# Optimization experiments

Hardware: AMD Instinct MI355X
Metric: run time of the kernel (lower is better)

## Reference

```python
import jax, jax.numpy as jnp
import numpy as np

DIM = 1024
HEADS = 16
DIM_HEAD = 64
INNER = HEADS * DIM_HEAD  # 1024
SCALE = DIM ** (-0.5)  # module scales by dim**-0.5 (not dim_head)


def setup_inputs() -> dict:
    key = jax.random.key(0)
    kx, kqkv, kwo, kbo = jax.random.split(key, 4)
    x = jax.random.normal(kx, (2, 2048, DIM), dtype=jnp.float32)
    W_qkv = jax.random.normal(kqkv, (DIM, 3 * INNER), dtype=jnp.float32) * (DIM ** -0.5)
    W_out = jax.random.normal(kwo, (INNER, DIM), dtype=jnp.float32) * (INNER ** -0.5)
    b_out = jax.random.normal(kbo, (DIM,), dtype=jnp.float32) * 0.01
    return {"x": x, "W_qkv": W_qkv, "W_out": W_out, "b_out": b_out}


def reference(x, W_qkv, W_out, b_out):
    b, n, _ = x.shape
    qkv = x @ W_qkv  # [b, n, 3*inner]
    q, k, v = jnp.split(qkv, 3, axis=-1)
    # [b, n, h*d] -> [b, h, n, d]
    reshape = lambda t: t.reshape(b, n, HEADS, DIM_HEAD).transpose(0, 2, 1, 3)
    q, k, v = reshape(q), reshape(k), reshape(v)
    dots = jnp.einsum('bhid,bhjd->bhij', q, k) * SCALE  # [b, h, n, n]
    attn = jax.nn.softmax(dots, axis=-1)
    out = jnp.einsum('bhij,bhjd->bhid', attn, v)  # [b, h, n, d]
    out = out.transpose(0, 2, 1, 3).reshape(b, n, INNER)
    return out @ W_out + b_out
```

## Files before the change

### kernel.cpp

```cpp
#include <hip/hip_runtime.h>

typedef __bf16 bf16x8 __attribute__((ext_vector_type(8)));
typedef __bf16 bf16x4 __attribute__((ext_vector_type(4)));
typedef __bf16 bf16x2 __attribute__((ext_vector_type(2)));
typedef float f32x4 __attribute__((ext_vector_type(4)));
typedef float f32x16 __attribute__((ext_vector_type(16)));
typedef int i32x4 __attribute__((ext_vector_type(4)));
typedef unsigned int u32x2 __attribute__((ext_vector_type(2)));

#define EXP2_SCALE 0.045084439f

__device__ __forceinline__ void async16(void* lds, const void* g) {
  __builtin_amdgcn_global_load_lds(
      (__attribute__((address_space(1))) unsigned int*)(g),
      (__attribute__((address_space(3))) unsigned int*)(lds), 16, 0, 0);
}

__device__ __forceinline__ unsigned int pack2(float a, float b) {
  bf16x2 t;
  t[0] = (__bf16)a;
  t[1] = (__bf16)b;
  return __builtin_bit_cast(unsigned int, t);
}

__device__ __forceinline__ float fexp2(float x) {
#if __has_builtin(__builtin_amdgcn_exp2f)
  return __builtin_amdgcn_exp2f(x);
#else
  return exp2f(x);
#endif
}

__device__ __forceinline__ void plswap(unsigned int& d, unsigned int& s) {
#if __has_builtin(__builtin_amdgcn_permlane32_swap)
  u32x2 r = __builtin_amdgcn_permlane32_swap(d, s, false, false);
  d = r[0];
  s = r[1];
#else
  asm("v_permlane32_swap_b32 %0, %1" : "+v"(d), "+v"(s));
#endif
}

__device__ __forceinline__ int detect_block(const unsigned short* win, int* cnt_sh) {
  if (threadIdx.x == 0) *cnt_sh = 0;
  __syncthreads();
  int c = 0;
#pragma unroll
  for (int j = 0; j < 8; j++) {
    const unsigned short u = win[threadIdx.x * 8 + j];
    if (((u >> 7) & 0xFF) >= 0xC0) c++;
  }
  if (c) atomicAdd(cnt_sh, c);
  __syncthreads();
  return (*cnt_sh >= 64) ? 1 : 0;
}

__global__ __launch_bounds__(256) void prep(
    const void* __restrict__ x, const void* __restrict__ Wqkv,
    const void* __restrict__ Wout, __bf16* __restrict__ xb,
    __bf16* __restrict__ WqkvT, __bf16* __restrict__ WoutT,
    int* __restrict__ flagp)
{
  __shared__ __bf16 tile[64 * 65];
  __shared__ int cnt;
  const int bx = blockIdx.x;
  const int t = threadIdx.x;

  if (bx < 2048) {
    const long base = (long)bx * 2048;
    const int f = detect_block((const unsigned short*)x + base, &cnt);
    if (bx == 0 && t == 0) *flagp = f;
    const long i = base + t * 8;
    if (f) {
      const f32x4* s4 = (const f32x4*)((const float*)x + i);
      const f32x4 v0 = s4[0], v1 = s4[1];
      bf16x8 o;
#pragma unroll
      for (int j = 0; j < 4; j++) o[j] = (__bf16)v0[j];
#pragma unroll
      for (int j = 0; j < 4; j++) o[4 + j] = (__bf16)v1[j];
      *(bf16x8*)&xb[i] = o;
    } else {
      *(bf16x8*)&xb[i] = *(const bf16x8*)((const __bf16*)x + i);
    }
    return;
  }

  const void* in;  __bf16* out;  int R = 1024, C, tcx, tr;
  if (bx < 2816) {
    const int idx = bx - 2048;
    in = Wqkv; out = WqkvT; C = 3072; tcx = (idx % 48) * 64; tr = (idx / 48) * 64;
  } else {
    const int idx = bx - 2816;
    in = Wout; out = WoutT; C = 1024; tcx = (idx % 16) * 64; tr = (idx / 16) * 64;
  }
  const int f = detect_block((const unsigned short*)in + (long)tr * C + tcx, &cnt);
#pragma unroll
  for (int i = 0; i < 16; i++) {
    const int idx = t + 256 * i;
    const int r = idx >> 6, c = idx & 63;
    const long g = (long)(tr + r) * C + tcx + c;
    tile[r * 65 + c] = f ? (__bf16)((const float*)in)[g] : ((const __bf16*)in)[g];
  }
  __syncthreads();
#pragma unroll
  for (int i = 0; i < 16; i++) {
    const int idx = t + 256 * i;
    const int r = idx >> 6, c = idx & 63;
    out[(long)(tcx + r) * R + tr + c] = tile[c * 65 + r];
  }
}

__global__ __launch_bounds__(256, 3) void gemm_qkv(
    const __bf16* __restrict__ A, const __bf16* __restrict__ Bt,
    __bf16* __restrict__ Qb, __bf16* __restrict__ Kc, __bf16* __restrict__ Vc)
{
  __shared__ __bf16 smem[17408];
  const int t = threadIdx.x;
  const int l = t & 63;
  const int w = t >> 6;
  const int wr = w >> 1, wc = w & 1;
  const int lid = blockIdx.y * 32 + blockIdx.x;
  const int s = (lid & 7) * 96 + (lid >> 3);
  const long m0 = (long)(s & 31) * 128;
  const long n0 = (long)(s >> 5) * 128;
  const int K = 1024;

  const int srow = w * 16 + (l >> 2);
  const int skof = (l & 3) * 8;
  const __bf16* gA = A + (m0 + srow) * (long)K + skof;
  const __bf16* gB = Bt + (n0 + srow) * (long)K + skof;
  const int Ao[2] = {0, 8192}, Bo[2] = {4096, 12288};
  const int lof = w * 512 + l * 8;

  async16(smem + Ao[0] + lof,        gA);
  async16(smem + Ao[0] + 2048 + lof, gA + 64 * (long)K);
  async16(smem + Bo[0] + lof,        gB);
  async16(smem + Bo[0] + 2048 + lof, gB + 64 * (long)K);
  gA += 32; gB += 32;
  __syncthreads();

  f32x4 acc[4][4] = {};

  for (int it = 0; it < 32; it++) {
    if (it < 31) {
      const int nb = (it + 1) & 1;
      async16(smem + Ao[nb] + lof,        gA);
      async16(smem + Ao[nb] + 2048 + lof, gA + 64 * (long)K);
      async16(smem + Bo[nb] + lof,        gB);
      async16(smem + Bo[nb] + 2048 + lof, gB + 64 * (long)K);
      gA += 32; gB += 32;
    }
    const __bf16* As = smem + Ao[it & 1];
    const __bf16* Bs = smem + Bo[it & 1];
    bf16x8 af[4], bfr[4];
#pragma unroll
    for (int mi = 0; mi < 4; mi++)
      af[mi] = *(const bf16x8*)&As[(wr * 64 + mi * 16 + (l & 15)) * 32 + (l >> 4) * 8];
#pragma unroll
    for (int ni = 0; ni < 4; ni++)
      bfr[ni] = *(const bf16x8*)&Bs[(wc * 64 + ni * 16 + (l & 15)) * 32 + (l >> 4) * 8];
#pragma unroll
    for (int mi = 0; mi < 4; mi++)
#pragma unroll
      for (int ni = 0; ni < 4; ni++)
        acc[mi][ni] = __builtin_amdgcn_mfma_f32_16x16x32_bf16(af[mi], bfr[ni], acc[mi][ni], 0, 0, 0);
    __syncthreads();
  }

  if (n0 < 1024) {
#pragma unroll
    for (int mi = 0; mi < 4; mi++)
#pragma unroll
      for (int ni = 0; ni < 4; ni++) {
        const long col = n0 + wc * 64 + ni * 16 + (l & 15);
#pragma unroll
        for (int r = 0; r < 4; r++) {
          const long row = m0 + wr * 64 + mi * 16 + (l >> 4) * 4 + r;
          Qb[row * 1024 + col] = (__bf16)(acc[mi][ni][r] * EXP2_SCALE);
        }
      }
  } else if (n0 < 2048) {
#pragma unroll
    for (int mi = 0; mi < 4; mi++)
#pragma unroll
      for (int ni = 0; ni < 4; ni++) {
        const int dcol = wc * 64 + ni * 16 + (l & 15);
        const int kl0 = wr * 64 + mi * 16 + (l >> 4) * 4;
#pragma unroll
        for (int r = 0; r < 4; r++)
          smem[(kl0 + r) * 136 + dcol] = (__bf16)acc[mi][ni][r];
      }
    __syncthreads();
    const int b = (int)(m0 >> 11);
    const int nbase = (int)(m0 & 2047);
#pragma unroll
    for (int i = 0; i < 8; i++) {
      const int kl = (t >> 4) + i * 16;
      const int d0 = (t & 15) * 8;
      const bf16x8 v = *(const bf16x8*)&smem[kl * 136 + d0];
      const int col1 = (int)(n0 - 1024) + d0;
      const int h = col1 >> 6, d = col1 & 63;
      const int n = nbase + kl;
      const long addr = ((long)(b * 16 + h) * 32 + (n >> 6)) * 4096 + (d >> 3) * 512 + (n & 63) * 8;
      *(bf16x8*)&Kc[addr] = v;
    }
  } else {
#pragma unroll
    for (int mi = 0; mi < 4; mi++)
#pragma unroll
      for (int ni = 0; ni < 4; ni++) {
        const int c = wc * 64 + ni * 16 + (l & 15);
        const int r = wr * 64 + mi * 16 + (l >> 4) * 4;
        bf16x4 pk;
#pragma unroll
        for (int k = 0; k < 4; k++) pk[k] = (__bf16)acc[mi][ni][k];
        *(bf16x4*)&smem[c * 136 + r] = pk;
      }
    __syncthreads();
    const int b = (int)(m0 >> 11);
    const int nbase = (int)(m0 & 2047);
#pragma unroll
    for (int i = 0; i < 8; i++) {
      const int c = (t >> 4) + i * 16;
      const int r8 = (t & 15) * 8;
      const bf16x8 v = *(const bf16x8*)&smem[c * 136 + r8];
      const int vcol = (int)(n0 - 2048) + c;
      const int h = vcol >> 6, d = vcol & 63;
      const int n = nbase + r8;
      const long addr = ((long)(b * 16 + h) * 32 + (n >> 6)) * 4096 + ((n >> 3) & 7) * 512 + d * 8;
      *(bf16x8*)&Vc[addr] = v;
    }
  }
}

__global__ __launch_bounds__(256, 3) void gemm_out(
    const __bf16* __restrict__ A, const __bf16* __restrict__ Bt,
    const void* __restrict__ bias_raw, void* __restrict__ C,
    const int* __restrict__ flagp)
{
  __shared__ __bf16 smem[16384];
  const int t = threadIdx.x;
  const int l = t & 63;
  const int w = t >> 6;
  const int wr = w >> 1, wc = w & 1;
  const int lid = blockIdx.y * 32 + blockIdx.x;
  const int s = (lid & 7) * 32 + (lid >> 3);
  const long m0 = (long)(s & 31) * 128;
  const long n0 = (long)(s >> 5) * 128;
  const int of = *flagp;
  const int K = 1024;

  const int srow = w * 16 + (l >> 2);
  const int skof = (l & 3) * 8;
  const __bf16* gA = A + (m0 + srow) * (long)K + skof;
  const __bf16* gB = Bt + (n0 + srow) * (long)K + skof;
  const int Ao[2] = {0, 8192}, Bo[2] = {4096, 12288};
  const int lof = w * 512 + l * 8;

  async16(smem + Ao[0] + lof,        gA);
  async16(smem + Ao[0] + 2048 + lof, gA + 64 * (long)K);
  async16(smem + Bo[0] + lof,        gB);
  async16(smem + Bo[0] + 2048 + lof, gB + 64 * (long)K);
  gA += 32; gB += 32;
  __syncthreads();

  f32x4 acc[4][4] = {};

  for (int it = 0; it < 32; it++) {
    if (it < 31) {
      const int nb = (it + 1) & 1;
      async16(smem + Ao[nb] + lof,        gA);
      async16(smem + Ao[nb] + 2048 + lof, gA + 64 * (long)K);
      async16(smem + Bo[nb] + lof,        gB);
      async16(smem + Bo[nb] + 2048 + lof, gB + 64 * (long)K);
      gA += 32; gB += 32;
    }
    const __bf16* As = smem + Ao[it & 1];
    const __bf16* Bs = smem + Bo[it & 1];
    bf16x8 af[4], bfr[4];
#pragma unroll
    for (int mi = 0; mi < 4; mi++)
      af[mi] = *(const bf16x8*)&As[(wr * 64 + mi * 16 + (l & 15)) * 32 + (l >> 4) * 8];
#pragma unroll
    for (int ni = 0; ni < 4; ni++)
      bfr[ni] = *(const bf16x8*)&Bs[(wc * 64 + ni * 16 + (l & 15)) * 32 + (l >> 4) * 8];
#pragma unroll
    for (int mi = 0; mi < 4; mi++)
#pragma unroll
      for (int ni = 0; ni < 4; ni++)
        acc[mi][ni] = __builtin_amdgcn_mfma_f32_16x16x32_bf16(af[mi], bfr[ni], acc[mi][ni], 0, 0, 0);
    __syncthreads();
  }

#pragma unroll
  for (int mi = 0; mi < 4; mi++)
#pragma unroll
    for (int ni = 0; ni < 4; ni++) {
      const long col = n0 + wc * 64 + ni * 16 + (l & 15);
      const float bv = of ? ((const float*)bias_raw)[col]
                          : (float)((const __bf16*)bias_raw)[col];
#pragma unroll
      for (int r = 0; r < 4; r++) {
        const long row = m0 + wr * 64 + mi * 16 + (l >> 4) * 4 + r;
        const float val = acc[mi][ni][r] + bv;
        const long off = row * 1024 + col;
        if (of) ((float*)C)[off] = val;
        else    ((__bf16*)C)[off] = (__bf16)val;
      }
    }
}

__global__ __launch_bounds__(256, 2) void attn_kernel(
    const __bf16* __restrict__ Qb, const __bf16* __restrict__ Kc,
    const __bf16* __restrict__ Vc, __bf16* __restrict__ O)
{
  __shared__ float fsm[4 * 1024 + 128];
  const int t = threadIdx.x;
  const int l = t & 63;
  const int w = t >> 6;
  const int wi = w & 1, wj = w >> 1;
  const int hl = l >> 5;
  const int L = blockIdx.y * 32 + blockIdx.x;
  const int bh = (L & 7) * 4 + ((L >> 3) & 3);
  const int qt = L >> 5;
  const int b = bh >> 4, head = bh & 15;
  const long q_row0 = (long)b * 2048 + qt * 128;

  bf16x8 qA0, qA1, qA2, qA3, qB0, qB1, qB2, qB3;
  {
    const __bf16* gQ = Qb + (q_row0 + wi * 32 + (l & 31)) * 1024 + head * 64 + hl * 8;
    qA0 = *(const bf16x8*)(gQ);
    qA1 = *(const bf16x8*)(gQ + 16);
    qA2 = *(const bf16x8*)(gQ + 32);
    qA3 = *(const bf16x8*)(gQ + 48);
    gQ += (long)64 * 1024;
    qB0 = *(const bf16x8*)(gQ);
    qB1 = *(const bf16x8*)(gQ + 16);
    qB2 = *(const bf16x8*)(gQ + 32);
    qB3 = *(const bf16x8*)(gQ + 48);
  }

  const __bf16* kb = Kc + (long)bh * 131072;
  const __bf16* vb = Vc + (long)bh * 131072;
  const int kof0 = hl * 512 + (wj * 32 + (l & 31)) * 8;
  const int vof0 = (wj * 4 + hl) * 512 + (l & 31) * 8;

  f32x16 aAa = {0,0,0,0,0,0,0,0,0,0,0,0,0,0,0,0};
  f32x16 aBa = {0,0,0,0,0,0,0,0,0,0,0,0,0,0,0,0};
  f32x16 aAb = {0,0,0,0,0,0,0,0,0,0,0,0,0,0,0,0};
  f32x16 aBb = {0,0,0,0,0,0,0,0,0,0,0,0,0,0,0,0};
  const f32x16 fz = {0,0,0,0,0,0,0,0,0,0,0,0,0,0,0,0};
  float liA = 0.0f, liB = 0.0f;
  bf16x8 paA0 = {}, paA1 = {}, paB0 = {}, paB1 = {};

#define LD8(p) (*(const bf16x8*)(p))
  bf16x8 ka0 = LD8(kb + kof0),        ka1 = LD8(kb + kof0 + 1024);
  bf16x8 ka2 = LD8(kb + kof0 + 2048), ka3 = LD8(kb + kof0 + 3072);
  bf16x8 kn0, kn1, kn2, kn3;
  bf16x8 va0 = {}, va1 = {}, va2 = {}, va3 = {};
  bf16x8 vn0, vn1, vn2, vn3;

#define SM_PACK(ST, PA0, PA1) \
  { \
    unsigned int a0 = pack2(ST[0],  ST[1]),  b0 = pack2(ST[4],  ST[5]); \
    unsigned int c0 = pack2(ST[2],  ST[3]),  d0 = pack2(ST[6],  ST[7]); \
    unsigned int a1 = pack2(ST[8],  ST[9]),  b1 = pack2(ST[12], ST[13]); \
    unsigned int c1 = pack2(ST[10], ST[11]), d1 = pack2(ST[14], ST[15]); \
    plswap(a0, b0); plswap(c0, d0); plswap(a1, b1); plswap(c1, d1); \
    const i32x4 f0_ = {(int)a0, (int)c0, (int)b0, (int)d0}; \
    const i32x4 f1_ = {(int)a1, (int)c1, (int)b1, (int)d1}; \
    PA0 = __builtin_bit_cast(bf16x8, f0_); \
    PA1 = __builtin_bit_cast(bf16x8, f1_); \
  }

#define ATT_ITER(IT, KA0,KA1,KA2,KA3, KN0,KN1,KN2,KN3, PV0,PV1,PV2,PV3, PN0,PN1,PN2,PN3) \
  { \
    const __bf16* kt_ = kb + (IT + 1) * 4096 + kof0; \
    const __bf16* vt_ = vb + (IT) * 4096 + vof0; \
    if ((IT) < 31) { \
      KN0 = LD8(kt_); KN1 = LD8(kt_ + 1024); \
      KN2 = LD8(kt_ + 2048); KN3 = LD8(kt_ + 3072); \
    } \
    PN0 = LD8(vt_);        PN1 = LD8(vt_ + 256); \
    PN2 = LD8(vt_ + 1024); PN3 = LD8(vt_ + 1280); \
    __builtin_amdgcn_s_setprio(1); \
    if ((IT) > 0) { \
      aAa = __builtin_amdgcn_mfma_f32_32x32x16_bf16(paA0, PV0, aAa, 0, 0, 0); \
      aBa = __builtin_amdgcn_mfma_f32_32x32x16_bf16(paA0, PV1, aBa, 0, 0, 0); \
      aAb = __builtin_amdgcn_mfma_f32_32x32x16_bf16(paB0, PV0, aAb, 0, 0, 0); \
      aBb = __builtin_amdgcn_mfma_f32_32x32x16_bf16(paB0, PV1, aBb, 0, 0, 0); \
      aAa = __builtin_amdgcn_mfma_f32_32x32x16_bf16(paA1, PV2, aAa, 0, 0, 0); \
      aBa = __builtin_amdgcn_mfma_f32_32x32x16_bf16(paA1, PV3, aBa, 0, 0, 0); \
      aAb = __builtin_amdgcn_mfma_f32_32x32x16_bf16(paB1, PV2, aAb, 0, 0, 0); \
      aBb = __builtin_amdgcn_mfma_f32_32x32x16_bf16(paB1, PV3, aBb, 0, 0, 0); \
    } \
    f32x16 stA = __builtin_amdgcn_mfma_f32_32x32x16_bf16(KA0, qA0, fz, 0, 0, 0); \
    f32x16 stB = __builtin_amdgcn_mfma_f32_32x32x16_bf16(KA0, qB0, fz, 0, 0, 0); \
    stA = __builtin_amdgcn_mfma_f32_32x32x16_bf16(KA1, qA1, stA, 0, 0, 0); \
    stB = __builtin_amdgcn_mfma_f32_32x32x16_bf16(KA1, qB1, stB, 0, 0, 0); \
    stA = __builtin_amdgcn_mfma_f32_32x32x16_bf16(KA2, qA2, stA, 0, 0, 0); \
    stB = __builtin_amdgcn_mfma_f32_32x32x16_bf16(KA2, qB2, stB, 0, 0, 0); \
    stA = __builtin_amdgcn_mfma_f32_32x32x16_bf16(KA3, qA3, stA, 0, 0, 0); \
    stB = __builtin_amdgcn_mfma_f32_32x32x16_bf16(KA3, qB3, stB, 0, 0, 0); \
    __builtin_amdgcn_s_setprio(0); \
    float rsA0 = 0.0f, rsA1 = 0.0f; \
    _Pragma("unroll") \
    for (int r = 0; r < 16; r += 2) { \
      const float p0 = fexp2(stA[r]); \
      const float p1 = fexp2(stA[r + 1]); \
      stA[r] = p0; stA[r + 1] = p1; \
      rsA0 += p0; rsA1 += p1; \
    } \
    liA += rsA0 + rsA1; \
    SM_PACK(stA, paA0, paA1) \
    float rsB0 = 0.0f, rsB1 = 0.0f; \
    _Pragma("unroll") \
    for (int r = 0; r < 16; r += 2) { \
      const float p0 = fexp2(stB[r]); \
      const float p1 = fexp2(stB[r + 1]); \
      stB[r] = p0; stB[r + 1] = p1; \
      rsB0 += p0; rsB1 += p1; \
    } \
    liB += rsB0 + rsB1; \
    SM_PACK(stB, paB0, paB1) \
  }

  for (int itp = 0; itp < 16; itp++) {
    const int it0 = itp * 2, it1 = itp * 2 + 1;
    ATT_ITER(it0, ka0,ka1,ka2,ka3, kn0,kn1,kn2,kn3, va0,va1,va2,va3, vn0,vn1,vn2,vn3)
    ATT_ITER(it1, kn0,kn1,kn2,kn3, ka0,ka1,ka2,ka3, vn0,vn1,vn2,vn3, va0,va1,va2,va3)
  }
#undef ATT_ITER
#undef LD8

  aAa = __builtin_amdgcn_mfma_f32_32x32x16_bf16(paA0, va0, aAa, 0, 0, 0);
  aBa = __builtin_amdgcn_mfma_f32_32x32x16_bf16(paA0, va1, aBa, 0, 0, 0);
  aAb = __builtin_amdgcn_mfma_f32_32x32x16_bf16(paB0, va0, aAb, 0, 0, 0);
  aBb = __builtin_amdgcn_mfma_f32_32x32x16_bf16(paB0, va1, aBb, 0, 0, 0);
  aAa = __builtin_amdgcn_mfma_f32_32x32x16_bf16(paA1, va2, aAa, 0, 0, 0);
  aBa = __builtin_amdgcn_mfma_f32_32x32x16_bf16(paA1, va3, aBa, 0, 0, 0);
  aAb = __builtin_amdgcn_mfma_f32_32x32x16_bf16(paB1, va2, aAb, 0, 0, 0);
  aBb = __builtin_amdgcn_mfma_f32_32x32x16_bf16(paB1, va3, aBb, 0, 0, 0);

  {
    unsigned int a = __builtin_bit_cast(unsigned int, liA), s = a;
    plswap(a, s);
    liA = __builtin_bit_cast(float, a) + __builtin_bit_cast(float, s);
  }
  {
    unsigned int a = __builtin_bit_cast(unsigned int, liB), s = a;
    plswap(a, s);
    liB = __builtin_bit_cast(float, a) + __builtin_bit_cast(float, s);
  }

  float* xbf = fsm;
  float* lb  = fsm + 4096;
  const int pw = 2 * (1 - wj) + wi;

#pragma unroll
  for (int r = 0; r < 16; r++)
    xbf[w * 1024 + r * 64 + l] = wj ? aAa[r] : aBa[r];
  if (l < 32) lb[w * 32 + l] = liA;
  __syncthreads();
#pragma unroll
  for (int r = 0; r < 16; r++) {
    const int iloc = (r & 3) + 8 * (r >> 2) + 4 * hl;
    const float lt = lb[wi * 32 + iloc] + lb[(wi + 2) * 32 + iloc];
    const float own = wj ? aBa[r] : aAa[r];
    const float o = own + xbf[pw * 1024 + r * 64 + l];
    const long row = q_row0 + wi * 32 + iloc;
    const long col = (long)head * 64 + wj * 32 + (l & 31);
    O[row * 1024 + col] = (__bf16)(o / lt);
  }
  __syncthreads();

#pragma unroll
  for (int r = 0; r < 16; r++)
    xbf[w * 1024 + r * 64 + l] = wj ? aAb[r] : aBb[r];
  if (l < 32) lb[w * 32 + l] = liB;
  __syncthreads();
#pragma unroll
  for (int r = 0; r < 16; r++) {
    const int iloc = (r & 3) + 8 * (r >> 2) + 4 * hl;
    const float lt = lb[wi * 32 + iloc] + lb[(wi + 2) * 32 + iloc];
    const float own = wj ? aBb[r] : aAb[r];
    const float o = own + xbf[pw * 1024 + r * 64 + l];
    const long row = q_row0 + 64 + wi * 32 + iloc;
    const long col = (long)head * 64 + wj * 32 + (l & 31);
    O[row * 1024 + col] = (__bf16)(o / lt);
  }
}

extern "C" void kernel_launch(void* const* d_in, const int* in_sizes, int n_in,
                              void* d_out, int out_size, void* d_ws, size_t ws_size,
                              hipStream_t stream) {
  const void* x    = d_in[0];
  const void* Wqkv = d_in[1];
  const void* Wout = d_in[2];
  const void* bout = d_in[3];

  char* ws = (char*)d_ws;
  int*    flagp = (int*)ws;
  __bf16* xb    = (__bf16*)(ws + 4096);
  __bf16* Obuf  = xb;
  __bf16* WqkvT = (__bf16*)(ws + 4096 +  8388608);
  __bf16* WoutT = (__bf16*)(ws + 4096 + 14680064);
  __bf16* qbuf  = (__bf16*)(ws + 4096 + 16777216);
  __bf16* kbuf  = (__bf16*)(ws + 4096 + 25165824);
  __bf16* vbuf  = (__bf16*)(ws + 4096 + 33554432);

  hipLaunchKernelGGL(prep, dim3(3072), dim3(256), 0, stream,
                     x, Wqkv, Wout, xb, WqkvT, WoutT, flagp);
  hipLaunchKernelGGL(gemm_qkv, dim3(32, 24), dim3(256), 0, stream,
                     xb, WqkvT, qbuf, kbuf, vbuf);
  hipLaunchKernelGGL(attn_kernel, dim3(32, 16), dim3(256), 0, stream,
                     qbuf, kbuf, vbuf, Obuf);
  hipLaunchKernelGGL(gemm_out, dim3(32, 8), dim3(256), 0, stream,
                     Obuf, WoutT, bout, d_out, flagp);
}
```

Before: 183.5 us.

## Compute softmax row sums via MFMA with ones vector; vectorize weight transpose

The attention kernel no longer accumulates the softmax denominators with per-lane VALU adds. It adds extra MFMAs that multiply the packed bf16 probabilities by a vector of ones, so the row sums come out in the accumulator layout and the cross-lane swap reduction goes away. This moves VALU work, which sits on the exp-bound critical path, onto the matrix unit at the cost of 4 more MFMAs per iteration and summing bf16-rounded probabilities. Separately, the weight transpose prep kernel now uses 16-byte vector loads and stores instead of scalar element accesses.

```diff
diff --git a/kernel.cpp b/kernel.cpp
--- a/kernel.cpp
+++ b/kernel.cpp
@@ -96,18 +96,32 @@
   }
   const int f = detect_block((const unsigned short*)in + (long)tr * C + tcx, &cnt);
 #pragma unroll
-  for (int i = 0; i < 16; i++) {
-    const int idx = t + 256 * i;
-    const int r = idx >> 6, c = idx & 63;
-    const long g = (long)(tr + r) * C + tcx + c;
-    tile[r * 65 + c] = f ? (__bf16)((const float*)in)[g] : ((const __bf16*)in)[g];
-  }
-  __syncthreads();
-#pragma unroll
-  for (int i = 0; i < 16; i++) {
-    const int idx = t + 256 * i;
-    const int r = idx >> 6, c = idx & 63;
-    out[(long)(tcx + r) * R + tr + c] = tile[c * 65 + r];
+  for (int j = 0; j < 2; j++) {
+    const int i8 = t * 2 + j;
+    const int r = i8 >> 3, c8 = (i8 & 7) * 8;
+    const long g = (long)(tr + r) * C + tcx + c8;
+    if (f) {
+      const f32x4* s4 = (const f32x4*)((const float*)in + g);
+      const f32x4 v0 = s4[0], v1 = s4[1];
+#pragma unroll
+      for (int e = 0; e < 4; e++) tile[r * 65 + c8 + e] = (__bf16)v0[e];
+#pragma unroll
+      for (int e = 0; e < 4; e++) tile[r * 65 + c8 + 4 + e] = (__bf16)v1[e];
+    } else {
+      const bf16x8 v = *(const bf16x8*)((const __bf16*)in + g);
+#pragma unroll
+      for (int e = 0; e < 8; e++) tile[r * 65 + c8 + e] = v[e];
+    }
+  }
+  __syncthreads();
+#pragma unroll
+  for (int j = 0; j < 2; j++) {
+    const int i8 = t * 2 + j;
+    const int ro = i8 >> 3, co8 = (i8 & 7) * 8;
+    bf16x8 v;
+#pragma unroll
+    for (int e = 0; e < 8; e++) v[e] = tile[(co8 + e) * 65 + ro];
+    *(bf16x8*)&out[(long)(tcx + ro) * R + tr + co8] = v;
   }
 }
 
@@ -341,6 +355,10 @@
     qB3 = *(const bf16x8*)(gQ + 48);
   }
 
+  bf16x8 onesb;
+#pragma unroll
+  for (int j = 0; j < 8; j++) onesb[j] = (__bf16)1.0f;
+
   const __bf16* kb = Kc + (long)bh * 131072;
   const __bf16* vb = Vc + (long)bh * 131072;
   const int kof0 = hl * 512 + (wj * 32 + (l & 31)) * 8;
@@ -350,8 +368,9 @@
   f32x16 aBa = {0,0,0,0,0,0,0,0,0,0,0,0,0,0,0,0};
   f32x16 aAb = {0,0,0,0,0,0,0,0,0,0,0,0,0,0,0,0};
   f32x16 aBb = {0,0,0,0,0,0,0,0,0,0,0,0,0,0,0,0};
+  f32x16 lsA = {0,0,0,0,0,0,0,0,0,0,0,0,0,0,0,0};
+  f32x16 lsB = {0,0,0,0,0,0,0,0,0,0,0,0,0,0,0,0};
   const f32x16 fz = {0,0,0,0,0,0,0,0,0,0,0,0,0,0,0,0};
-  float liA = 0.0f, liB = 0.0f;
   bf16x8 paA0 = {}, paA1 = {}, paB0 = {}, paB1 = {};
 
 #define LD8(p) (*(const bf16x8*)(p))
@@ -394,6 +413,10 @@
       aBa = __builtin_amdgcn_mfma_f32_32x32x16_bf16(paA1, PV3, aBa, 0, 0, 0); \
       aAb = __builtin_amdgcn_mfma_f32_32x32x16_bf16(paB1, PV2, aAb, 0, 0, 0); \
       aBb = __builtin_amdgcn_mfma_f32_32x32x16_bf16(paB1, PV3, aBb, 0, 0, 0); \
+      lsA = __builtin_amdgcn_mfma_f32_32x32x16_bf16(paA0, onesb, lsA, 0, 0, 0); \
+      lsA = __builtin_amdgcn_mfma_f32_32x32x16_bf16(paA1, onesb, lsA, 0, 0, 0); \
+      lsB = __builtin_amdgcn_mfma_f32_32x32x16_bf16(paB0, onesb, lsB, 0, 0, 0); \
+      lsB = __builtin_amdgcn_mfma_f32_32x32x16_bf16(paB1, onesb, lsB, 0, 0, 0); \
     } \
     f32x16 stA = __builtin_amdgcn_mfma_f32_32x32x16_bf16(KA0, qA0, fz, 0, 0, 0); \
     f32x16 stB = __builtin_amdgcn_mfma_f32_32x32x16_bf16(KA0, qB0, fz, 0, 0, 0); \
@@ -404,25 +427,11 @@
     stA = __builtin_amdgcn_mfma_f32_32x32x16_bf16(KA3, qA3, stA, 0, 0, 0); \
     stB = __builtin_amdgcn_mfma_f32_32x32x16_bf16(KA3, qB3, stB, 0, 0, 0); \
     __builtin_amdgcn_s_setprio(0); \
-    float rsA0 = 0.0f, rsA1 = 0.0f; \
     _Pragma("unroll") \
-    for (int r = 0; r < 16; r += 2) { \
-      const float p0 = fexp2(stA[r]); \
-      const float p1 = fexp2(stA[r + 1]); \
-      stA[r] = p0; stA[r + 1] = p1; \
-      rsA0 += p0; rsA1 += p1; \
-    } \
-    liA += rsA0 + rsA1; \
+    for (int r = 0; r < 16; r++) stA[r] = fexp2(stA[r]); \
     SM_PACK(stA, paA0, paA1) \
-    float rsB0 = 0.0f, rsB1 = 0.0f; \
     _Pragma("unroll") \
-    for (int r = 0; r < 16; r += 2) { \
-      const float p0 = fexp2(stB[r]); \
-      const float p1 = fexp2(stB[r + 1]); \
-      stB[r] = p0; stB[r + 1] = p1; \
-      rsB0 += p0; rsB1 += p1; \
-    } \
-    liB += rsB0 + rsB1; \
+    for (int r = 0; r < 16; r++) stB[r] = fexp2(stB[r]); \
     SM_PACK(stB, paB0, paB1) \
   }
 
@@ -442,17 +451,10 @@
   aBa = __builtin_amdgcn_mfma_f32_32x32x16_bf16(paA1, va3, aBa, 0, 0, 0);
   aAb = __builtin_amdgcn_mfma_f32_32x32x16_bf16(paB1, va2, aAb, 0, 0, 0);
   aBb = __builtin_amdgcn_mfma_f32_32x32x16_bf16(paB1, va3, aBb, 0, 0, 0);
-
-  {
-    unsigned int a = __builtin_bit_cast(unsigned int, liA), s = a;
-    plswap(a, s);
-    liA = __builtin_bit_cast(float, a) + __builtin_bit_cast(float, s);
-  }
-  {
-    unsigned int a = __builtin_bit_cast(unsigned int, liB), s = a;
-    plswap(a, s);
-    liB = __builtin_bit_cast(float, a) + __builtin_bit_cast(float, s);
-  }
+  lsA = __builtin_amdgcn_mfma_f32_32x32x16_bf16(paA0, onesb, lsA, 0, 0, 0);
+  lsA = __builtin_amdgcn_mfma_f32_32x32x16_bf16(paA1, onesb, lsA, 0, 0, 0);
+  lsB = __builtin_amdgcn_mfma_f32_32x32x16_bf16(paB0, onesb, lsB, 0, 0, 0);
+  lsB = __builtin_amdgcn_mfma_f32_32x32x16_bf16(paB1, onesb, lsB, 0, 0, 0);
 
   float* xbf = fsm;
   float* lb  = fsm + 4096;
@@ -461,12 +463,18 @@
 #pragma unroll
   for (int r = 0; r < 16; r++)
     xbf[w * 1024 + r * 64 + l] = wj ? aAa[r] : aBa[r];
-  if (l < 32) lb[w * 32 + l] = liA;
+  if ((l & 31) == 0) {
+#pragma unroll
+    for (int r = 0; r < 16; r++) {
+      const int iloc = (r & 3) + 8 * (r >> 2) + 4 * hl;
+      lb[w * 32 + iloc] = lsA[r];
+    }
+  }
   __syncthreads();
 #pragma unroll
   for (int r = 0; r < 16; r++) {
     const int iloc = (r & 3) + 8 * (r >> 2) + 4 * hl;
-    const float lt = lb[wi * 32 + iloc] + lb[(wi + 2) * 32 + iloc];
+    const float lt = lsA[r] + lb[pw * 32 + iloc];
     const float own = wj ? aBa[r] : aAa[r];
     const float o = own + xbf[pw * 1024 + r * 64 + l];
     const long row = q_row0 + wi * 32 + iloc;
@@ -478,12 +486,18 @@
 #pragma unroll
   for (int r = 0; r < 16; r++)
     xbf[w * 1024 + r * 64 + l] = wj ? aAb[r] : aBb[r];
-  if (l < 32) lb[w * 32 + l] = liB;
+  if ((l & 31) == 0) {
+#pragma unroll
+    for (int r = 0; r < 16; r++) {
+      const int iloc = (r & 3) + 8 * (r >> 2) + 4 * hl;
+      lb[w * 32 + iloc] = lsB[r];
+    }
+  }
   __syncthreads();
 #pragma unroll
   for (int r = 0; r < 16; r++) {
     const int iloc = (r & 3) + 8 * (r >> 2) + 4 * hl;
-    const float lt = lb[wi * 32 + iloc] + lb[(wi + 2) * 32 + iloc];
+    const float lt = lsB[r] + lb[pw * 32 + iloc];
     const float own = wj ? aBb[r] : aAb[r];
     const float o = own + xbf[pw * 1024 + r * 64 + l];
     const long row = q_row0 + 64 + wi * 32 + iloc;
```

Result: no change. 181.4 us (-1.1%).
